# Kernel optimization log

Hardware: AMD Instinct MI355X
Metric: run time of the kernel (lower is better)

## Reference

```python
import jax, jax.numpy as jnp
import numpy as np

N, BS, DIM, SIZE = 512, 64, 256, 8192

def setup_inputs() -> dict:
    key = jax.random.key(0)
    k1, k2 = jax.random.split(key)
    seq = jax.random.normal(k1, (N, BS, DIM), dtype=jnp.float32)
    # codebook initialized Uniform[-1, 1] as in _reset_parameters
    vocab = jax.random.uniform(k2, (SIZE, DIM), dtype=jnp.float32, minval=-1.0, maxval=1.0)
    return {"seq": seq, "vocab": vocab}

def reference(seq, vocab):
    n, bs, d = seq.shape
    x = seq.reshape(n * bs, d)                                   # [T, D]
    # squared euclidean distances; argmin identical to cdist(p=2).argmin
    x2 = jnp.sum(x * x, axis=-1, keepdims=True)                  # [T, 1]
    v2 = jnp.sum(vocab * vocab, axis=-1)                         # [K]
    d2 = x2 - 2.0 * (x @ vocab.T) + v2                           # [T, K]
    ingredients = jnp.argmin(d2, axis=1)                          # [T]
    out = jnp.take(vocab, ingredients, axis=0).reshape(n, bs, d)  # quantized seq
    return out, ingredients.reshape(n, bs)
```

## Files before the change

### kernel.cpp

```cpp
#include <hip/hip_runtime.h>

#define T_TOTAL 32768
#define D       256
#define K       8192
#define BQ      64
#define KSPLIT  4
#define KSLICE  (K / KSPLIT)
#define NSLICE  (KSPLIT * 4)
#define NCT     (K / 16)
#define KT_STRIDE (NCT * 64 * 8)
#define NQB     (T_TOTAL / BQ)

typedef _Float16 half4f  __attribute__((ext_vector_type(4)));
typedef _Float16 half8f  __attribute__((ext_vector_type(8)));
typedef float    floatx4 __attribute__((ext_vector_type(4)));

#define PARTIAL_F 1048576
#define BHALVES   2097152

__device__ __forceinline__ _Float16 hi16(float x) { return (_Float16)x; }
__device__ __forceinline__ _Float16 lo16(float x, _Float16 h) { return (_Float16)(x - (float)h); }
__device__ __forceinline__ void split4(float4 v, half4f& h, half4f& l) {
    _Float16 hx = hi16(v.x), hy = hi16(v.y), hz = hi16(v.z), hw = hi16(v.w);
    h = (half4f){hx, hy, hz, hw};
    l = (half4f){lo16(v.x, hx), lo16(v.y, hy), lo16(v.z, hz), lo16(v.w, hw)};
}

__global__ void prep_kernel(const float* __restrict__ vocab,
                            _Float16* __restrict__ bhi, _Float16* __restrict__ blo,
                            float* __restrict__ hv2) {
    const int ct = blockIdx.x;
    const int t  = threadIdx.x;
    const int k4 = t & 63;
    const int w  = t >> 6;
    const float4* voc4 = (const float4*)vocab;
    const int kt = k4 >> 3, kg = (k4 >> 1) & 3, h = k4 & 1;
    float ss[4];
    #pragma unroll
    for (int ci = 0; ci < 4; ++ci) {
        int cc = w * 4 + ci;
        float4 v = voc4[(size_t)(ct * 16 + cc) * (D / 4) + k4];
        half4f hh, ll;
        split4(v, hh, ll);
        size_t off = (((size_t)kt * NCT + ct) * 64 + (cc + 16 * kg)) * 8 + h * 4;
        *(half4f*)&bhi[off] = hh;
        *(half4f*)&blo[off] = ll;
        ss[ci] = v.x * v.x + v.y * v.y + v.z * v.z + v.w * v.w;
    }
    #pragma unroll
    for (int ci = 0; ci < 4; ++ci) {
        float s = ss[ci];
        #pragma unroll
        for (int off = 32; off; off >>= 1) s += __shfl_down(s, off, 64);
        if ((t & 63) == 0) hv2[ct * 16 + w * 4 + ci] = 0.5f * s;
    }
}

__launch_bounds__(256, 2)
__global__ void argmin_kernel(const float* __restrict__ seq,
                              const _Float16* __restrict__ bhi,
                              const _Float16* __restrict__ blo,
                              const float* __restrict__ hv2,
                              float2* __restrict__ partial) {
    __shared__ _Float16 AhL[4 * 8 * 64 * 8];
    __shared__ _Float16 AlL[4 * 8 * 64 * 8];

    const int t    = threadIdx.x;
    const int lane = t & 63;
    const int wn   = t >> 6;
    const int bi   = blockIdx.x;
    const int slice = (bi & 7) >> 1;
    const int qb    = (bi >> 3) * 2 + (bi & 1);
    const int q0   = qb * BQ;
    const int k0   = slice * KSLICE;

    const float4* seq4 = (const float4*)seq;

    #pragma unroll
    for (int i = 0; i < 16; ++i) {
        int f   = t + 256 * i;
        int row = f >> 6;
        int d4  = f & 63;
        float4 v = seq4[(size_t)(q0 + row) * (D / 4) + d4];
        half4f h, l;
        split4(v, h, l);
        int kt = d4 >> 3, kg = (d4 >> 1) & 3, hh = d4 & 1;
        int off = (((((row >> 4) * 8 + kt) * 64) + ((row & 15) + 16 * kg)) * 8 + hh * 4)
                  ^ (kt << 3);
        *(half4f*)&AhL[off] = h;
        *(half4f*)&AlL[off] = l;
    }
    __syncthreads();

    float best[16];
    int   bidx[16];
    #pragma unroll
    for (int b = 0; b < 16; ++b) { best[b] = 3.4e38f; bidx[b] = 0; }

    const _Float16* bh_l = bhi + (size_t)lane * 8;
    const _Float16* bl_l = blo + (size_t)lane * 8;

    for (int c0i = 0; c0i < KSLICE / 256; ++c0i) {
        const int c0  = k0 + c0i * 256;
        const int ct0 = (c0 >> 4) + wn * 4;
        const size_t cb = (size_t)ct0 * 512;

        floatx4 acc[4][4];
        #pragma unroll
        for (int mi = 0; mi < 4; ++mi)
            #pragma unroll
            for (int nj = 0; nj < 4; ++nj) acc[mi][nj] = (floatx4){0.f, 0.f, 0.f, 0.f};

        half8f bh0[4], bl0[4], bh1[4], bl1[4];
        half8f ah0[4], al0[4], ah1[4], al1[4];
        #pragma unroll
        for (int nj = 0; nj < 4; ++nj) {
            bh0[nj] = *(const half8f*)&bh_l[cb + nj * 512];
            bl0[nj] = *(const half8f*)&bl_l[cb + nj * 512];
        }
        #pragma unroll
        for (int mi = 0; mi < 4; ++mi) {
            const int ao = ((mi * 8) * 64 + lane) * 8;
            ah0[mi] = *(const half8f*)&AhL[ao];
            al0[mi] = *(const half8f*)&AlL[ao];
        }

        #pragma unroll 1
        for (int kt2 = 0; kt2 < 4; ++kt2) {
            const int kt = kt2 * 2;
            {
                const size_t kb = (size_t)(kt + 1) * KT_STRIDE + cb;
                #pragma unroll
                for (int nj = 0; nj < 4; ++nj) {
                    bh1[nj] = *(const half8f*)&bh_l[kb + nj * 512];
                    bl1[nj] = *(const half8f*)&bl_l[kb + nj * 512];
                }
                #pragma unroll
                for (int mi = 0; mi < 4; ++mi) {
                    const int ao = (((mi * 8 + kt + 1) * 64 + lane) * 8) ^ ((kt + 1) << 3);
                    ah1[mi] = *(const half8f*)&AhL[ao];
                    al1[mi] = *(const half8f*)&AlL[ao];
                }
            }
            #pragma unroll
            for (int nj = 0; nj < 4; ++nj)
                #pragma unroll
                for (int mi = 0; mi < 4; ++mi) {
                    floatx4 a = acc[mi][nj];
                    a = __builtin_amdgcn_mfma_f32_16x16x32_f16(al0[mi], bh0[nj], a, 0, 0, 0);
                    a = __builtin_amdgcn_mfma_f32_16x16x32_f16(ah0[mi], bl0[nj], a, 0, 0, 0);
                    a = __builtin_amdgcn_mfma_f32_16x16x32_f16(ah0[mi], bh0[nj], a, 0, 0, 0);
                    acc[mi][nj] = a;
                }
            if (kt2 < 3) {
                const size_t kb = (size_t)(kt + 2) * KT_STRIDE + cb;
                #pragma unroll
                for (int nj = 0; nj < 4; ++nj) {
                    bh0[nj] = *(const half8f*)&bh_l[kb + nj * 512];
                    bl0[nj] = *(const half8f*)&bl_l[kb + nj * 512];
                }
                #pragma unroll
                for (int mi = 0; mi < 4; ++mi) {
                    const int ao = (((mi * 8 + kt + 2) * 64 + lane) * 8) ^ ((kt + 2) << 3);
                    ah0[mi] = *(const half8f*)&AhL[ao];
                    al0[mi] = *(const half8f*)&AlL[ao];
                }
            }
            #pragma unroll
            for (int nj = 0; nj < 4; ++nj)
                #pragma unroll
                for (int mi = 0; mi < 4; ++mi) {
                    floatx4 a = acc[mi][nj];
                    a = __builtin_amdgcn_mfma_f32_16x16x32_f16(al1[mi], bh1[nj], a, 0, 0, 0);
                    a = __builtin_amdgcn_mfma_f32_16x16x32_f16(ah1[mi], bl1[nj], a, 0, 0, 0);
                    a = __builtin_amdgcn_mfma_f32_16x16x32_f16(ah1[mi], bh1[nj], a, 0, 0, 0);
                    acc[mi][nj] = a;
                }
        }

        #pragma unroll
        for (int nj = 0; nj < 4; ++nj) {
            int c = c0 + (wn * 4 + nj) * 16 + (lane & 15);
            float hv = hv2[c];
            #pragma unroll
            for (int mi = 0; mi < 4; ++mi)
                #pragma unroll
                for (int r = 0; r < 4; ++r) {
                    float s = hv - acc[mi][nj][r];
                    int b = mi * 4 + r;
                    if (s < best[b]) { best[b] = s; bidx[b] = c; }
                }
        }
    }

    #pragma unroll
    for (int off = 1; off < 16; off <<= 1) {
        #pragma unroll
        for (int b = 0; b < 16; ++b) {
            float ob = __shfl_xor(best[b], off, 64);
            int   oi = __shfl_xor(bidx[b], off, 64);
            if (ob < best[b] || (ob == best[b] && oi < bidx[b])) {
                best[b] = ob; bidx[b] = oi;
            }
        }
    }
    if ((lane & 15) == 0) {
        const size_t sl = (size_t)(slice * 4 + wn) * T_TOTAL;
        #pragma unroll
        for (int mi = 0; mi < 4; ++mi)
            #pragma unroll
            for (int r = 0; r < 4; ++r) {
                int q = q0 + mi * 16 + (lane >> 4) * 4 + r;
                partial[sl + q] = make_float2(best[mi * 4 + r], (float)bidx[mi * 4 + r]);
            }
    }
}

__global__ void redgather_kernel(const float* __restrict__ vocab,
                                 const float2* __restrict__ partial,
                                 float* __restrict__ out) {
    int r    = blockIdx.x * 4 + (threadIdx.x >> 6);
    int lane = threadIdx.x & 63;
    float bm = 3.4e38f;
    int   bi = 0x7fffffff;
    if (lane < 16) {
        float2 p = partial[(size_t)lane * T_TOTAL + r];
        bm = p.x; bi = (int)p.y;
    }
    #pragma unroll
    for (int off = 1; off < 16; off <<= 1) {
        float ob = __shfl_xor(bm, off, 64);
        int   oi = __shfl_xor(bi, off, 64);
        if (ob < bm || (ob == bm && oi < bi)) { bm = ob; bi = oi; }
    }
    int k = __shfl(bi, 0, 64);
    const float4* src = (const float4*)(vocab + (size_t)k * D);
    float4*       dst = (float4*)(out + (size_t)r * D);
    dst[lane] = src[lane];
    if (lane == 0) out[(size_t)T_TOTAL * D + r] = (float)k;
}

__global__ void reduce_kernel(const float2* __restrict__ partial, int* __restrict__ idx) {
    int q = blockIdx.x * 256 + threadIdx.x;
    float bm = 3.4e38f;
    int   bi = 0x7fffffff;
    #pragma unroll
    for (int s = 0; s < NSLICE; ++s) {
        float2 p = partial[(size_t)s * T_TOTAL + q];
        int pi = (int)p.y;
        if (p.x < bm || (p.x == bm && pi < bi)) { bm = p.x; bi = pi; }
    }
    idx[q] = bi;
}

__global__ void gather_kernel(const float* __restrict__ vocab,
                              const int* __restrict__ idx,
                              float* __restrict__ out) {
    int r    = blockIdx.x * 4 + (threadIdx.x >> 6);
    int lane = threadIdx.x & 63;
    int k = idx[r];
    const float4* src = (const float4*)(vocab + (size_t)k * D);
    float4*       dst = (float4*)(out + (size_t)r * D);
    dst[lane] = src[lane];
    if (lane == 0) out[(size_t)T_TOTAL * D + r] = (float)k;
}

extern "C" void kernel_launch(void* const* d_in, const int* in_sizes, int n_in,
                              void* d_out, int out_size, void* d_ws, size_t ws_size,
                              hipStream_t stream) {
    const float* seq   = (const float*)d_in[0];
    const float* vocab = (const float*)d_in[1];
    float* out = (float*)d_out;

    float* hv2 = (float*)d_ws;
    _Float16* bhi = (_Float16*)(out + PARTIAL_F);
    _Float16* blo = bhi + BHALVES;

    const size_t need_ws = (size_t)(K + 2 * NSLICE * T_TOTAL) * sizeof(float) + 256;
    const bool fused = ws_size >= need_ws;

    hipLaunchKernelGGL(prep_kernel, dim3(NCT), dim3(256), 0, stream, vocab, bhi, blo, hv2);

    if (fused) {
        float2* partial = (float2*)(hv2 + K);
        hipLaunchKernelGGL(argmin_kernel,    dim3(NQB * KSPLIT), dim3(256), 0, stream,
                           seq, bhi, blo, hv2, partial);
        hipLaunchKernelGGL(redgather_kernel, dim3(T_TOTAL / 4),  dim3(256), 0, stream,
                           vocab, partial, out);
    } else {
        float2* partial = (float2*)d_out;
        int* idx = (int*)(hv2 + K);
        hipLaunchKernelGGL(argmin_kernel, dim3(NQB * KSPLIT), dim3(256), 0, stream,
                           seq, bhi, blo, hv2, partial);
        hipLaunchKernelGGL(reduce_kernel, dim3(T_TOTAL / 256), dim3(256), 0, stream, partial, idx);
        hipLaunchKernelGGL(gather_kernel, dim3(T_TOTAL / 4),   dim3(256), 0, stream, vocab, idx, out);
    }
}
```

Before: 439.2 us.

## Switch distance GEMM to 32x32x16 MFMA tiles with matching operand layouts

Replaces the 16x16x32 f16 MFMA tiling (4x4 tiles per wave) with 32x32x16 MFMA (2x2 tiles per wave). The vocab prep layout and the shared-memory layout for the query tile are rearranged to match the new operand format. The argmin epilogue, cross-lane reduction and partial-result writes are adapted to the 16-element accumulators. The larger instruction is meant to cut operand loads and issue overhead per flop. In exchange there are more live accumulator and best/index registers, and the larger shuffle reduction may reduce occupancy.

```diff
diff --git a/kernel.cpp b/kernel.cpp
--- a/kernel.cpp
+++ b/kernel.cpp
@@ -7,13 +7,13 @@
 #define KSPLIT  4
 #define KSLICE  (K / KSPLIT)
 #define NSLICE  (KSPLIT * 4)
-#define NCT     (K / 16)
-#define KT_STRIDE (NCT * 64 * 8)
+#define NCT32   (K / 32)
+#define KT_STRIDE (NCT32 * 64 * 8)
 #define NQB     (T_TOTAL / BQ)
 
-typedef _Float16 half4f  __attribute__((ext_vector_type(4)));
-typedef _Float16 half8f  __attribute__((ext_vector_type(8)));
-typedef float    floatx4 __attribute__((ext_vector_type(4)));
+typedef _Float16 half4f   __attribute__((ext_vector_type(4)));
+typedef _Float16 half8f   __attribute__((ext_vector_type(8)));
+typedef float    floatx16 __attribute__((ext_vector_type(16)));
 
 #define PARTIAL_F 1048576
 #define BHALVES   2097152
@@ -34,25 +34,28 @@
     const int k4 = t & 63;
     const int w  = t >> 6;
     const float4* voc4 = (const float4*)vocab;
-    const int kt = k4 >> 3, kg = (k4 >> 1) & 3, h = k4 & 1;
-    float ss[4];
-    #pragma unroll
-    for (int ci = 0; ci < 4; ++ci) {
-        int cc = w * 4 + ci;
-        float4 v = voc4[(size_t)(ct * 16 + cc) * (D / 4) + k4];
+    const int kt = k4 >> 2;
+    const int q  = k4 & 3;
+    const int fl = 32 * (q >> 1);
+    const int i0 = (q & 1) * 4;
+    float ss[8];
+    #pragma unroll
+    for (int ci = 0; ci < 8; ++ci) {
+        int cc = w * 8 + ci;
+        float4 v = voc4[(size_t)(ct * 32 + cc) * (D / 4) + k4];
         half4f hh, ll;
         split4(v, hh, ll);
-        size_t off = (((size_t)kt * NCT + ct) * 64 + (cc + 16 * kg)) * 8 + h * 4;
+        size_t off = (((size_t)kt * NCT32 + ct) * 64 + (cc + fl)) * 8 + i0;
         *(half4f*)&bhi[off] = hh;
         *(half4f*)&blo[off] = ll;
         ss[ci] = v.x * v.x + v.y * v.y + v.z * v.z + v.w * v.w;
     }
     #pragma unroll
-    for (int ci = 0; ci < 4; ++ci) {
+    for (int ci = 0; ci < 8; ++ci) {
         float s = ss[ci];
         #pragma unroll
         for (int off = 32; off; off >>= 1) s += __shfl_down(s, off, 64);
-        if ((t & 63) == 0) hv2[ct * 16 + w * 4 + ci] = 0.5f * s;
+        if ((t & 63) == 0) hv2[ct * 32 + w * 8 + ci] = 0.5f * s;
     }
 }
 
@@ -62,8 +65,8 @@
                               const _Float16* __restrict__ blo,
                               const float* __restrict__ hv2,
                               float2* __restrict__ partial) {
-    __shared__ _Float16 AhL[4 * 8 * 64 * 8];
-    __shared__ _Float16 AlL[4 * 8 * 64 * 8];
+    __shared__ _Float16 AhL[2 * 16 * 64 * 8];
+    __shared__ _Float16 AlL[2 * 16 * 64 * 8];
 
     const int t    = threadIdx.x;
     const int lane = t & 63;
@@ -84,119 +87,132 @@
         float4 v = seq4[(size_t)(q0 + row) * (D / 4) + d4];
         half4f h, l;
         split4(v, h, l);
-        int kt = d4 >> 3, kg = (d4 >> 1) & 3, hh = d4 & 1;
-        int off = (((((row >> 4) * 8 + kt) * 64) + ((row & 15) + 16 * kg)) * 8 + hh * 4)
+        int kt = d4 >> 2, qq = d4 & 3;
+        int off = (((((row >> 5) * 16 + kt) * 64) + ((row & 31) + 32 * (qq >> 1))) * 8
+                   + (qq & 1) * 4)
                   ^ (kt << 3);
         *(half4f*)&AhL[off] = h;
         *(half4f*)&AlL[off] = l;
     }
     __syncthreads();
 
-    float best[16];
-    int   bidx[16];
-    #pragma unroll
-    for (int b = 0; b < 16; ++b) { best[b] = 3.4e38f; bidx[b] = 0; }
+    float best[32];
+    int   bidx[32];
+    #pragma unroll
+    for (int b = 0; b < 32; ++b) { best[b] = 3.4e38f; bidx[b] = 0; }
 
     const _Float16* bh_l = bhi + (size_t)lane * 8;
     const _Float16* bl_l = blo + (size_t)lane * 8;
 
     for (int c0i = 0; c0i < KSLICE / 256; ++c0i) {
         const int c0  = k0 + c0i * 256;
-        const int ct0 = (c0 >> 4) + wn * 4;
+        const int ct0 = (c0 >> 5) + wn * 2;
         const size_t cb = (size_t)ct0 * 512;
 
-        floatx4 acc[4][4];
-        #pragma unroll
-        for (int mi = 0; mi < 4; ++mi)
-            #pragma unroll
-            for (int nj = 0; nj < 4; ++nj) acc[mi][nj] = (floatx4){0.f, 0.f, 0.f, 0.f};
-
-        half8f bh0[4], bl0[4], bh1[4], bl1[4];
-        half8f ah0[4], al0[4], ah1[4], al1[4];
-        #pragma unroll
-        for (int nj = 0; nj < 4; ++nj) {
+        floatx16 acc[2][2];
+        #pragma unroll
+        for (int mi = 0; mi < 2; ++mi)
+            #pragma unroll
+            for (int nj = 0; nj < 2; ++nj)
+                #pragma unroll
+                for (int r = 0; r < 16; ++r) acc[mi][nj][r] = 0.0f;
+
+        half8f bh0[2], bl0[2], bh1[2], bl1[2];
+        half8f ah0[2], al0[2], ah1[2], al1[2];
+        #pragma unroll
+        for (int nj = 0; nj < 2; ++nj) {
             bh0[nj] = *(const half8f*)&bh_l[cb + nj * 512];
             bl0[nj] = *(const half8f*)&bl_l[cb + nj * 512];
         }
         #pragma unroll
-        for (int mi = 0; mi < 4; ++mi) {
-            const int ao = ((mi * 8) * 64 + lane) * 8;
+        for (int mi = 0; mi < 2; ++mi) {
+            const int ao = ((mi * 16) * 64 + lane) * 8;
             ah0[mi] = *(const half8f*)&AhL[ao];
             al0[mi] = *(const half8f*)&AlL[ao];
         }
 
         #pragma unroll 1
-        for (int kt2 = 0; kt2 < 4; ++kt2) {
+        for (int kt2 = 0; kt2 < 8; ++kt2) {
             const int kt = kt2 * 2;
             {
                 const size_t kb = (size_t)(kt + 1) * KT_STRIDE + cb;
                 #pragma unroll
-                for (int nj = 0; nj < 4; ++nj) {
+                for (int nj = 0; nj < 2; ++nj) {
                     bh1[nj] = *(const half8f*)&bh_l[kb + nj * 512];
                     bl1[nj] = *(const half8f*)&bl_l[kb + nj * 512];
                 }
                 #pragma unroll
-                for (int mi = 0; mi < 4; ++mi) {
-                    const int ao = (((mi * 8 + kt + 1) * 64 + lane) * 8) ^ ((kt + 1) << 3);
+                for (int mi = 0; mi < 2; ++mi) {
+                    const int ao = (((mi * 16 + kt + 1) * 64 + lane) * 8) ^ ((kt + 1) << 3);
                     ah1[mi] = *(const half8f*)&AhL[ao];
                     al1[mi] = *(const half8f*)&AlL[ao];
                 }
             }
             #pragma unroll
-            for (int nj = 0; nj < 4; ++nj)
-                #pragma unroll
-                for (int mi = 0; mi < 4; ++mi) {
-                    floatx4 a = acc[mi][nj];
-                    a = __builtin_amdgcn_mfma_f32_16x16x32_f16(al0[mi], bh0[nj], a, 0, 0, 0);
-                    a = __builtin_amdgcn_mfma_f32_16x16x32_f16(ah0[mi], bl0[nj], a, 0, 0, 0);
-                    a = __builtin_amdgcn_mfma_f32_16x16x32_f16(ah0[mi], bh0[nj], a, 0, 0, 0);
-                    acc[mi][nj] = a;
-                }
-            if (kt2 < 3) {
+            for (int nj = 0; nj < 2; ++nj)
+                #pragma unroll
+                for (int mi = 0; mi < 2; ++mi)
+                    acc[mi][nj] = __builtin_amdgcn_mfma_f32_32x32x16_f16(al0[mi], bh0[nj], acc[mi][nj], 0, 0, 0);
+            #pragma unroll
+            for (int nj = 0; nj < 2; ++nj)
+                #pragma unroll
+                for (int mi = 0; mi < 2; ++mi)
+                    acc[mi][nj] = __builtin_amdgcn_mfma_f32_32x32x16_f16(ah0[mi], bl0[nj], acc[mi][nj], 0, 0, 0);
+            #pragma unroll
+            for (int nj = 0; nj < 2; ++nj)
+                #pragma unroll
+                for (int mi = 0; mi < 2; ++mi)
+                    acc[mi][nj] = __builtin_amdgcn_mfma_f32_32x32x16_f16(ah0[mi], bh0[nj], acc[mi][nj], 0, 0, 0);
+            if (kt2 < 7) {
                 const size_t kb = (size_t)(kt + 2) * KT_STRIDE + cb;
                 #pragma unroll
-                for (int nj = 0; nj < 4; ++nj) {
+                for (int nj = 0; nj < 2; ++nj) {
                     bh0[nj] = *(const half8f*)&bh_l[kb + nj * 512];
                     bl0[nj] = *(const half8f*)&bl_l[kb + nj * 512];
                 }
                 #pragma unroll
-                for (int mi = 0; mi < 4; ++mi) {
-                    const int ao = (((mi * 8 + kt + 2) * 64 + lane) * 8) ^ ((kt + 2) << 3);
+                for (int mi = 0; mi < 2; ++mi) {
+                    const int ao = (((mi * 16 + kt + 2) * 64 + lane) * 8) ^ ((kt + 2) << 3);
                     ah0[mi] = *(const half8f*)&AhL[ao];
                     al0[mi] = *(const half8f*)&AlL[ao];
                 }
             }
             #pragma unroll
-            for (int nj = 0; nj < 4; ++nj)
-                #pragma unroll
-                for (int mi = 0; mi < 4; ++mi) {
-                    floatx4 a = acc[mi][nj];
-                    a = __builtin_amdgcn_mfma_f32_16x16x32_f16(al1[mi], bh1[nj], a, 0, 0, 0);
-                    a = __builtin_amdgcn_mfma_f32_16x16x32_f16(ah1[mi], bl1[nj], a, 0, 0, 0);
-                    a = __builtin_amdgcn_mfma_f32_16x16x32_f16(ah1[mi], bh1[nj], a, 0, 0, 0);
-                    acc[mi][nj] = a;
-                }
-        }
-
-        #pragma unroll
-        for (int nj = 0; nj < 4; ++nj) {
-            int c = c0 + (wn * 4 + nj) * 16 + (lane & 15);
+            for (int nj = 0; nj < 2; ++nj)
+                #pragma unroll
+                for (int mi = 0; mi < 2; ++mi)
+                    acc[mi][nj] = __builtin_amdgcn_mfma_f32_32x32x16_f16(al1[mi], bh1[nj], acc[mi][nj], 0, 0, 0);
+            #pragma unroll
+            for (int nj = 0; nj < 2; ++nj)
+                #pragma unroll
+                for (int mi = 0; mi < 2; ++mi)
+                    acc[mi][nj] = __builtin_amdgcn_mfma_f32_32x32x16_f16(ah1[mi], bl1[nj], acc[mi][nj], 0, 0, 0);
+            #pragma unroll
+            for (int nj = 0; nj < 2; ++nj)
+                #pragma unroll
+                for (int mi = 0; mi < 2; ++mi)
+                    acc[mi][nj] = __builtin_amdgcn_mfma_f32_32x32x16_f16(ah1[mi], bh1[nj], acc[mi][nj], 0, 0, 0);
+        }
+
+        #pragma unroll
+        for (int nj = 0; nj < 2; ++nj) {
+            int c = c0 + (wn * 2 + nj) * 32 + (lane & 31);
             float hv = hv2[c];
             #pragma unroll
-            for (int mi = 0; mi < 4; ++mi)
-                #pragma unroll
-                for (int r = 0; r < 4; ++r) {
+            for (int mi = 0; mi < 2; ++mi)
+                #pragma unroll
+                for (int r = 0; r < 16; ++r) {
                     float s = hv - acc[mi][nj][r];
-                    int b = mi * 4 + r;
+                    int b = mi * 16 + r;
                     if (s < best[b]) { best[b] = s; bidx[b] = c; }
                 }
         }
     }
 
     #pragma unroll
-    for (int off = 1; off < 16; off <<= 1) {
-        #pragma unroll
-        for (int b = 0; b < 16; ++b) {
+    for (int off = 1; off < 32; off <<= 1) {
+        #pragma unroll
+        for (int b = 0; b < 32; ++b) {
             float ob = __shfl_xor(best[b], off, 64);
             int   oi = __shfl_xor(bidx[b], off, 64);
             if (ob < best[b] || (ob == best[b] && oi < bidx[b])) {
@@ -204,14 +220,15 @@
             }
         }
     }
-    if ((lane & 15) == 0) {
+    if ((lane & 31) == 0) {
         const size_t sl = (size_t)(slice * 4 + wn) * T_TOTAL;
-        #pragma unroll
-        for (int mi = 0; mi < 4; ++mi)
-            #pragma unroll
-            for (int r = 0; r < 4; ++r) {
-                int q = q0 + mi * 16 + (lane >> 4) * 4 + r;
-                partial[sl + q] = make_float2(best[mi * 4 + r], (float)bidx[mi * 4 + r]);
+        const int rowadd = (lane >> 5) * 4;
+        #pragma unroll
+        for (int mi = 0; mi < 2; ++mi)
+            #pragma unroll
+            for (int r = 0; r < 16; ++r) {
+                int qr = q0 + mi * 32 + (r & 3) + 8 * (r >> 2) + rowadd;
+                partial[sl + qr] = make_float2(best[mi * 16 + r], (float)bidx[mi * 16 + r]);
             }
     }
 }
@@ -279,7 +296,7 @@
     const size_t need_ws = (size_t)(K + 2 * NSLICE * T_TOTAL) * sizeof(float) + 256;
     const bool fused = ws_size >= need_ws;
 
-    hipLaunchKernelGGL(prep_kernel, dim3(NCT), dim3(256), 0, stream, vocab, bhi, blo, hv2);
+    hipLaunchKernelGGL(prep_kernel, dim3(NCT32), dim3(256), 0, stream, vocab, bhi, blo, hv2);
 
     if (fused) {
         float2* partial = (float2*)(hv2 + K);
```

New measurement: 480.4 us. 1.09x slower.

## Use 512-thread blocks with narrower per-wave tiles and fold wave results in LDS

Applied to the files above, without the earlier changes.

The argmin kernel now launches 8 waves per block instead of 4. Each wave computes 2 column tiles instead of 4, and the software double-buffering of operands is dropped in favour of a simple per-kt load-then-MFMA loop bracketed by s_setprio. Best indices are packed two per 32-bit register to cut register use, and the two halves of the block are merged through LDS before the partial results are written. The goal is higher occupancy and more latency hiding from extra waves, at the cost of losing explicit prefetch, adding block barriers, and relying on indices fitting in 16 bits.

```diff
diff --git a/kernel.cpp b/kernel.cpp
--- a/kernel.cpp
+++ b/kernel.cpp
@@ -56,7 +56,7 @@
     }
 }
 
-__launch_bounds__(256, 2)
+__attribute__((amdgpu_flat_work_group_size(512, 512), amdgpu_waves_per_eu(4)))
 __global__ void argmin_kernel(const float* __restrict__ seq,
                               const _Float16* __restrict__ bhi,
                               const _Float16* __restrict__ blo,
@@ -77,8 +77,8 @@
     const float4* seq4 = (const float4*)seq;
 
     #pragma unroll
-    for (int i = 0; i < 16; ++i) {
-        int f   = t + 256 * i;
+    for (int i = 0; i < 8; ++i) {
+        int f   = t + 512 * i;
         int row = f >> 6;
         int d4  = f & 63;
         float4 v = seq4[(size_t)(q0 + row) * (D / 4) + d4];
@@ -92,106 +92,86 @@
     }
     __syncthreads();
 
-    float best[16];
-    int   bidx[16];
-    #pragma unroll
-    for (int b = 0; b < 16; ++b) { best[b] = 3.4e38f; bidx[b] = 0; }
+    float    best[16];
+    unsigned bidxp[8];
+    #pragma unroll
+    for (int b = 0; b < 16; ++b) best[b] = 3.4e38f;
+    #pragma unroll
+    for (int b = 0; b < 8; ++b) bidxp[b] = 0u;
 
     const _Float16* bh_l = bhi + (size_t)lane * 8;
     const _Float16* bl_l = blo + (size_t)lane * 8;
 
     for (int c0i = 0; c0i < KSLICE / 256; ++c0i) {
         const int c0  = k0 + c0i * 256;
-        const int ct0 = (c0 >> 4) + wn * 4;
+        const int ct0 = (c0 >> 4) + wn * 2;
         const size_t cb = (size_t)ct0 * 512;
 
-        floatx4 acc[4][4];
+        floatx4 acc[4][2];
         #pragma unroll
         for (int mi = 0; mi < 4; ++mi)
             #pragma unroll
-            for (int nj = 0; nj < 4; ++nj) acc[mi][nj] = (floatx4){0.f, 0.f, 0.f, 0.f};
-
-        half8f bh0[4], bl0[4], bh1[4], bl1[4];
-        half8f ah0[4], al0[4], ah1[4], al1[4];
-        #pragma unroll
-        for (int nj = 0; nj < 4; ++nj) {
-            bh0[nj] = *(const half8f*)&bh_l[cb + nj * 512];
-            bl0[nj] = *(const half8f*)&bl_l[cb + nj * 512];
+            for (int nj = 0; nj < 2; ++nj) acc[mi][nj] = (floatx4){0.f, 0.f, 0.f, 0.f};
+
+        #pragma unroll 1
+        for (int kt = 0; kt < 8; ++kt) {
+            const size_t kb = (size_t)kt * KT_STRIDE + cb;
+            half8f bh[2], bl[2], ah[4], al[4];
+            #pragma unroll
+            for (int nj = 0; nj < 2; ++nj) {
+                bh[nj] = *(const half8f*)&bh_l[kb + nj * 512];
+                bl[nj] = *(const half8f*)&bl_l[kb + nj * 512];
+            }
+            #pragma unroll
+            for (int mi = 0; mi < 4; ++mi) {
+                const int ao = (((mi * 8 + kt) * 64 + lane) * 8) ^ (kt << 3);
+                ah[mi] = *(const half8f*)&AhL[ao];
+                al[mi] = *(const half8f*)&AlL[ao];
+            }
+            __builtin_amdgcn_s_setprio(1);
+            #pragma unroll
+            for (int nj = 0; nj < 2; ++nj)
+                #pragma unroll
+                for (int mi = 0; mi < 4; ++mi)
+                    acc[mi][nj] = __builtin_amdgcn_mfma_f32_16x16x32_f16(al[mi], bh[nj], acc[mi][nj], 0, 0, 0);
+            #pragma unroll
+            for (int nj = 0; nj < 2; ++nj)
+                #pragma unroll
+                for (int mi = 0; mi < 4; ++mi)
+                    acc[mi][nj] = __builtin_amdgcn_mfma_f32_16x16x32_f16(ah[mi], bl[nj], acc[mi][nj], 0, 0, 0);
+            #pragma unroll
+            for (int nj = 0; nj < 2; ++nj)
+                #pragma unroll
+                for (int mi = 0; mi < 4; ++mi)
+                    acc[mi][nj] = __builtin_amdgcn_mfma_f32_16x16x32_f16(ah[mi], bh[nj], acc[mi][nj], 0, 0, 0);
+            __builtin_amdgcn_s_setprio(0);
         }
-        #pragma unroll
-        for (int mi = 0; mi < 4; ++mi) {
-            const int ao = ((mi * 8) * 64 + lane) * 8;
-            ah0[mi] = *(const half8f*)&AhL[ao];
-            al0[mi] = *(const half8f*)&AlL[ao];
-        }
-
-        #pragma unroll 1
-        for (int kt2 = 0; kt2 < 4; ++kt2) {
-            const int kt = kt2 * 2;
-            {
-                const size_t kb = (size_t)(kt + 1) * KT_STRIDE + cb;
-                #pragma unroll
-                for (int nj = 0; nj < 4; ++nj) {
-                    bh1[nj] = *(const half8f*)&bh_l[kb + nj * 512];
-                    bl1[nj] = *(const half8f*)&bl_l[kb + nj * 512];
-                }
-                #pragma unroll
-                for (int mi = 0; mi < 4; ++mi) {
-                    const int ao = (((mi * 8 + kt + 1) * 64 + lane) * 8) ^ ((kt + 1) << 3);
-                    ah1[mi] = *(const half8f*)&AhL[ao];
-                    al1[mi] = *(const half8f*)&AlL[ao];
-                }
-            }
-            #pragma unroll
-            for (int nj = 0; nj < 4; ++nj)
-                #pragma unroll
-                for (int mi = 0; mi < 4; ++mi) {
-                    floatx4 a = acc[mi][nj];
-                    a = __builtin_amdgcn_mfma_f32_16x16x32_f16(al0[mi], bh0[nj], a, 0, 0, 0);
-                    a = __builtin_amdgcn_mfma_f32_16x16x32_f16(ah0[mi], bl0[nj], a, 0, 0, 0);
-                    a = __builtin_amdgcn_mfma_f32_16x16x32_f16(ah0[mi], bh0[nj], a, 0, 0, 0);
-                    acc[mi][nj] = a;
-                }
-            if (kt2 < 3) {
-                const size_t kb = (size_t)(kt + 2) * KT_STRIDE + cb;
-                #pragma unroll
-                for (int nj = 0; nj < 4; ++nj) {
-                    bh0[nj] = *(const half8f*)&bh_l[kb + nj * 512];
-                    bl0[nj] = *(const half8f*)&bl_l[kb + nj * 512];
-                }
-                #pragma unroll
-                for (int mi = 0; mi < 4; ++mi) {
-                    const int ao = (((mi * 8 + kt + 2) * 64 + lane) * 8) ^ ((kt + 2) << 3);
-                    ah0[mi] = *(const half8f*)&AhL[ao];
-                    al0[mi] = *(const half8f*)&AlL[ao];
-                }
-            }
-            #pragma unroll
-            for (int nj = 0; nj < 4; ++nj)
-                #pragma unroll
-                for (int mi = 0; mi < 4; ++mi) {
-                    floatx4 a = acc[mi][nj];
-                    a = __builtin_amdgcn_mfma_f32_16x16x32_f16(al1[mi], bh1[nj], a, 0, 0, 0);
-                    a = __builtin_amdgcn_mfma_f32_16x16x32_f16(ah1[mi], bl1[nj], a, 0, 0, 0);
-                    a = __builtin_amdgcn_mfma_f32_16x16x32_f16(ah1[mi], bh1[nj], a, 0, 0, 0);
-                    acc[mi][nj] = a;
+
+        #pragma unroll
+        for (int nj = 0; nj < 2; ++nj) {
+            const int c = c0 + (wn * 2 + nj) * 16 + (lane & 15);
+            const float hv = hv2[c];
+            const unsigned clo = (unsigned)c;
+            const unsigned chi = (unsigned)c << 16;
+            #pragma unroll
+            for (int mi = 0; mi < 4; ++mi)
+                #pragma unroll
+                for (int r = 0; r < 4; r += 2) {
+                    const int b = mi * 4 + r;
+                    float s0 = hv - acc[mi][nj][r];
+                    float s1 = hv - acc[mi][nj][r + 1];
+                    unsigned w = bidxp[b >> 1];
+                    if (s0 < best[b])     { best[b] = s0;     w = (w & 0xFFFF0000u) | clo; }
+                    if (s1 < best[b + 1]) { best[b + 1] = s1; w = (w & 0x0000FFFFu) | chi; }
+                    bidxp[b >> 1] = w;
                 }
         }
-
-        #pragma unroll
-        for (int nj = 0; nj < 4; ++nj) {
-            int c = c0 + (wn * 4 + nj) * 16 + (lane & 15);
-            float hv = hv2[c];
-            #pragma unroll
-            for (int mi = 0; mi < 4; ++mi)
-                #pragma unroll
-                for (int r = 0; r < 4; ++r) {
-                    float s = hv - acc[mi][nj][r];
-                    int b = mi * 4 + r;
-                    if (s < best[b]) { best[b] = s; bidx[b] = c; }
-                }
-        }
-    }
+    }
+
+    int bidx[16];
+    #pragma unroll
+    for (int b = 0; b < 16; ++b)
+        bidx[b] = (b & 1) ? (int)(bidxp[b >> 1] >> 16) : (int)(bidxp[b >> 1] & 0xFFFFu);
 
     #pragma unroll
     for (int off = 1; off < 16; off <<= 1) {
@@ -204,14 +184,34 @@
             }
         }
     }
-    if ((lane & 15) == 0) {
+
+    float2* fold = (float2*)AhL;
+    __syncthreads();
+    if (wn >= 4 && (lane & 15) == 0) {
+        #pragma unroll
+        for (int mi = 0; mi < 4; ++mi)
+            #pragma unroll
+            for (int r = 0; r < 4; ++r) {
+                int row = mi * 16 + (lane >> 4) * 4 + r;
+                fold[(wn - 4) * 64 + row] =
+                    make_float2(best[mi * 4 + r], (float)bidx[mi * 4 + r]);
+            }
+    }
+    __syncthreads();
+    if (wn < 4 && (lane & 15) == 0) {
         const size_t sl = (size_t)(slice * 4 + wn) * T_TOTAL;
         #pragma unroll
         for (int mi = 0; mi < 4; ++mi)
             #pragma unroll
             for (int r = 0; r < 4; ++r) {
-                int q = q0 + mi * 16 + (lane >> 4) * 4 + r;
-                partial[sl + q] = make_float2(best[mi * 4 + r], (float)bidx[mi * 4 + r]);
+                int row = mi * 16 + (lane >> 4) * 4 + r;
+                int b = mi * 4 + r;
+                float2 p = fold[wn * 64 + row];
+                int pi = (int)p.y;
+                if (p.x < best[b] || (p.x == best[b] && pi < bidx[b])) {
+                    best[b] = p.x; bidx[b] = pi;
+                }
+                partial[sl + q0 + row] = make_float2(best[b], (float)bidx[b]);
             }
     }
 }
@@ -283,14 +283,14 @@
 
     if (fused) {
         float2* partial = (float2*)(hv2 + K);
-        hipLaunchKernelGGL(argmin_kernel,    dim3(NQB * KSPLIT), dim3(256), 0, stream,
+        hipLaunchKernelGGL(argmin_kernel,    dim3(NQB * KSPLIT), dim3(512), 0, stream,
                            seq, bhi, blo, hv2, partial);
         hipLaunchKernelGGL(redgather_kernel, dim3(T_TOTAL / 4),  dim3(256), 0, stream,
                            vocab, partial, out);
     } else {
         float2* partial = (float2*)d_out;
         int* idx = (int*)(hv2 + K);
-        hipLaunchKernelGGL(argmin_kernel, dim3(NQB * KSPLIT), dim3(256), 0, stream,
+        hipLaunchKernelGGL(argmin_kernel, dim3(NQB * KSPLIT), dim3(512), 0, stream,
                            seq, bhi, blo, hv2, partial);
         hipLaunchKernelGGL(reduce_kernel, dim3(T_TOTAL / 256), dim3(256), 0, stream, partial, idx);
         hipLaunchKernelGGL(gather_kernel, dim3(T_TOTAL / 4),   dim3(256), 0, stream, vocab, idx, out);
```

After: 446.3 us. Within noise of the previous version (+1.6%).
